# Kernel optimization log

Measured on AMD Instinct MI355X. Metric: run time of the kernel, lower is better.

## Reference

```python
import jax, jax.numpy as jnp
import numpy as np

B, N, L, C, K = 2, 8192, 8192, 128, 8
RADIUS = 0.4

def _gather(t, idx):
    # t: [B,L,D], idx: [B,N,K] -> [B,N,K,D]
    b, n, k = idx.shape
    return jnp.take_along_axis(t, idx.reshape(b, n * k)[:, :, None], axis=1).reshape(b, n, k, t.shape[-1])

def _ln(x, g, b):
    m = x.mean(-1, keepdims=True)
    v = x.var(-1, keepdims=True)
    return (x - m) * jax.lax.rsqrt(v + 1e-5) * g + b

def setup_inputs() -> dict:
    key = jax.random.key(0)
    ks = jax.random.split(key, 16)
    F = 4 * C
    def w(k, i, o):
        return jax.random.normal(k, (i, o), jnp.float32) / np.sqrt(i).astype(np.float32)
    return {
        "q_xyz": jax.random.uniform(ks[0], (B, N, 3), jnp.float32),
        "q_feat": jax.random.normal(ks[1], (B, N, C), jnp.float32),
        "kv_xyz": jax.random.uniform(ks[2], (B, L, 3), jnp.float32),
        "kv_feat": jax.random.normal(ks[3], (B, L, C), jnp.float32),
        "kv_pad": jnp.zeros((B, L), bool),
        "pos_w1": w(ks[4], 3, C), "pos_b1": jnp.zeros((C,), jnp.float32),
        "pos_w2": w(ks[5], C, C), "pos_b2": jnp.zeros((C,), jnp.float32),
        "attn_w": w(ks[6], C, C), "attn_b": jnp.zeros((C,), jnp.float32),
        "lin_w": w(ks[7], C, C),
        "lin_src_w": w(ks[8], C, C),
        "lin_dst_w": w(ks[9], C, C),
        "ln1_g": jnp.ones((C,), jnp.float32), "ln1_b": jnp.zeros((C,), jnp.float32),
        "ffn_w1": w(ks[10], C, F), "ffn_b1": jnp.zeros((F,), jnp.float32),
        "ffn_w2": w(ks[11], F, C), "ffn_b2": jnp.zeros((C,), jnp.float32),
        "ln2_g": jnp.ones((C,), jnp.float32), "ln2_b": jnp.zeros((C,), jnp.float32),
    }

def reference(q_xyz, q_feat, kv_xyz, kv_feat, kv_pad,
              pos_w1, pos_b1, pos_w2, pos_b2, attn_w, attn_b,
              lin_w, lin_src_w, lin_dst_w, ln1_g, ln1_b,
              ffn_w1, ffn_b1, ffn_w2, ffn_b2, ln2_g, ln2_b):
    # --- radius graph: up to K nearest kv points within RADIUS per query ---
    d2 = jnp.sum((q_xyz[:, :, None, :] - kv_xyz[:, None, :, :]) ** 2, -1)  # [B,N,L]
    ok = (d2 <= RADIUS ** 2) & (~kv_pad)[:, None, :]
    neg_d2, idx = jax.lax.top_k(jnp.where(ok, -d2, -jnp.inf), K)  # [B,N,K]
    ev = jnp.isfinite(neg_d2)  # edge-valid mask [B,N,K]

    # --- PointTransformerConv (vector attention, per-edge) ---
    pos_j = _gather(kv_xyz, idx)                           # [B,N,K,3]
    rel = q_xyz[:, :, None, :] - pos_j                     # pos_i - pos_j
    # pos_nn: MLP([3,C,C], plain_last=False) => ReLU after each Linear
    delta = jax.nn.relu(jax.nn.relu(rel @ pos_w1 + pos_b1) @ pos_w2 + pos_b2)  # [B,N,K,C]
    a_src = _gather(kv_feat @ lin_src_w, idx)              # [B,N,K,C]
    a_dst = q_feat @ lin_dst_w                             # [B,N,C]
    x_j = _gather(kv_feat @ lin_w, idx)                    # [B,N,K,C]
    # attn_nn: MLP([C,C], plain_last=False) => Linear + ReLU
    alpha = jax.nn.relu((a_dst[:, :, None, :] - a_src + delta) @ attn_w + attn_b)
    # segment softmax over the K neighbors (invalid edges masked out)
    scores = jnp.where(ev[..., None], alpha, -jnp.inf)
    mx = jnp.max(scores, axis=2, keepdims=True)
    mx = jnp.where(jnp.isfinite(mx), mx, 0.0)
    e = jnp.where(ev[..., None], jnp.exp(scores - mx), 0.0)
    attn = e / jnp.maximum(e.sum(2, keepdims=True), 1e-12)
    agg = jnp.sum(attn * (x_j + delta), axis=2)            # [B,N,C]

    # --- residual + LN + FFN + LN (dropout = identity at eval) ---
    out = _ln(q_feat + agg, ln1_g, ln1_b)
    h = jax.nn.gelu(out @ ffn_w1 + ffn_b1, approximate=False) @ ffn_w2 + ffn_b2
    return _ln(out + h, ln2_g, ln2_b)
```

## Files before the change

kernel.cpp:

```cpp
#include <hip/hip_runtime.h>
#include <math.h>

#define NB 2
#define NQ 8192
#define NL 8192
#define NC 128
#define NKN 8
#define NF 512
#define MQ (NB*NQ)

typedef __attribute__((ext_vector_type(8))) short bf16x8;
typedef __attribute__((ext_vector_type(4))) float f32x4;

__device__ __forceinline__ unsigned short f2bf_u(float f){
    unsigned u = __float_as_uint(f);
    return (unsigned short)((u + 0x7FFFu + ((u>>16)&1u)) >> 16);
}
__device__ __forceinline__ float bf2f(unsigned short s){
    return __uint_as_float(((unsigned)s) << 16);
}


__device__ __forceinline__ int cell_coord(float x) {
    int c = (int)(x * 16.0f);
    return min(15, max(0, c));
}

__global__ __launch_bounds__(256) void grid_count_kernel(
    const float* __restrict__ kxyz, const unsigned char* __restrict__ pad,
    int* __restrict__ cnt)
{
    int t = blockIdx.x*256 + threadIdx.x;
    if (pad[t]) return;
    int bat = t >> 13;
    float x = kxyz[t*3+0], y = kxyz[t*3+1], z = kxyz[t*3+2];
    int cell = (cell_coord(z)*16 + cell_coord(y))*16 + cell_coord(x);
    atomicAdd(&cnt[bat*4096 + cell], 1);
}

__global__ __launch_bounds__(1024) void grid_scan_kernel(
    const int* __restrict__ cnt, int* __restrict__ cs)
{
    __shared__ int wsum[17];
    int t = threadIdx.x;
    int v[8]; int s = 0;
    #pragma unroll
    for (int k = 0; k < 8; ++k) { v[k] = s; s += cnt[t*8 + k]; }
    int lane = t & 63, w = t >> 6;
    int inc = s;
    #pragma unroll
    for (int d = 1; d < 64; d <<= 1) {
        int o = __shfl_up(inc, d);
        if (lane >= d) inc += o;
    }
    if (lane == 63) wsum[w] = inc;
    __syncthreads();
    if (t == 0) {
        int a = 0;
        for (int i = 0; i < 16; ++i) { int x = wsum[i]; wsum[i] = a; a += x; }
        wsum[16] = a;
    }
    __syncthreads();
    int base = wsum[w] + (inc - s);
    #pragma unroll
    for (int k = 0; k < 8; ++k) cs[t*8 + k] = base + v[k];
    if (t == 1023) cs[8192] = wsum[16];
}

__global__ __launch_bounds__(256) void grid_scatter_kernel(
    const float* __restrict__ kxyz, const unsigned char* __restrict__ pad,
    const int* __restrict__ cs, int* __restrict__ fill, float4* __restrict__ ro)
{
    int t = blockIdx.x*256 + threadIdx.x;
    if (pad[t]) return;
    int bat = t >> 13, i = t & 8191;
    float x = kxyz[t*3+0], y = kxyz[t*3+1], z = kxyz[t*3+2];
    int cell = bat*4096 + (cell_coord(z)*16 + cell_coord(y))*16 + cell_coord(x);
    int pos = cs[cell] + atomicAdd(&fill[cell], 1);
    ro[pos] = make_float4(x, y, z, __int_as_float(i));
}

__device__ __forceinline__ void insert8(float cd, int id, float dk[8], int ik[8]) {
    if (cd < dk[7]) {
        dk[7] = cd; ik[7] = id;
        #pragma unroll
        for (int r = 6; r >= 0; --r) {
            bool sw = dk[r+1] < dk[r];
            float td = dk[r]; int ti = ik[r];
            dk[r]   = sw ? dk[r+1] : dk[r];
            ik[r]   = sw ? ik[r+1] : ik[r];
            dk[r+1] = sw ? td : dk[r+1];
            ik[r+1] = sw ? ti : ik[r+1];
        }
    }
}

template<int W>
__device__ __forceinline__ void scan_block(int l, int cx, int cy, int cz,
    float qx, float qy, float qz, const int* __restrict__ CS,
    const float4* __restrict__ RO, float dk[8], int ik[8])
{
    const int D = 2*W + 1;
    int xs = max(0, cx - W), xe = min(15, cx + W);
    int nx = xe - xs + 1;
    for (int r = l; r < D*D; r += 8) {
        int dz = r / D - W, dy = r % D - W;
        int zz = cz + dz, yy = cy + dy;
        if ((unsigned)zz > 15u || (unsigned)yy > 15u) continue;
        int c0 = (zz*16 + yy)*16 + xs;
        int s = CS[c0], e = CS[c0 + nx];
        for (int p = s; p < e; ++p) {
            float4 v = RO[p];
            float dx = qx - v.x, dyv = qy - v.y, dzv = qz - v.z;
            float cd = dx*dx + dyv*dyv + dzv*dzv;
            insert8(cd, __float_as_int(v.w), dk, ik);
        }
    }
}

__device__ __forceinline__ void merge8(float dk[8], int ik[8]) {
    #pragma unroll
    for (int m = 1; m <= 4; m <<= 1) {
        float od[8]; int oi[8];
        #pragma unroll
        for (int r = 0; r < 8; ++r) {
            od[r] = __shfl_xor(dk[r], m);
            oi[r] = __shfl_xor(ik[r], m);
        }
        float nd[8]; int ni[8];
        #pragma unroll
        for (int r = 0; r < 8; ++r) {
            bool take = od[7-r] < dk[r];
            nd[r] = take ? od[7-r] : dk[r];
            ni[r] = take ? oi[7-r] : ik[r];
        }
        #pragma unroll
        for (int st = 4; st >= 1; st >>= 1) {
            #pragma unroll
            for (int r = 0; r < 8; ++r) {
                if ((r & st) == 0 && (r | st) < 8) {
                    int b = r | st;
                    bool sw = nd[b] < nd[r];
                    float td = nd[r]; int ti = ni[r];
                    nd[r] = sw ? nd[b] : nd[r];
                    ni[r] = sw ? ni[b] : ni[r];
                    nd[b] = sw ? td : nd[b];
                    ni[b] = sw ? ti : ni[b];
                }
            }
        }
        #pragma unroll
        for (int r = 0; r < 8; ++r) { dk[r] = nd[r]; ik[r] = ni[r]; }
    }
}

__global__ __launch_bounds__(256) void radius_grid_query_kernel(
    const float* __restrict__ qxyz, const int* __restrict__ cellstart,
    const float4* __restrict__ reorder, int* __restrict__ idxout)
{
    const int tid  = threadIdx.x;
    const int l    = tid & 7;
    const int qloc = tid >> 3;
    const int gq   = blockIdx.x*32 + qloc;
    const int bat  = gq >> 13;
    const float qx = qxyz[gq*3+0], qy = qxyz[gq*3+1], qz = qxyz[gq*3+2];
    const int cx = cell_coord(qx), cy = cell_coord(qy), cz = cell_coord(qz);
    const int* CS = cellstart + bat*4096;
    const float R2  = (float)(0.4*0.4);
    const float R2P = __uint_as_float(__float_as_uint(R2) + 1u);

    float dk[8]; int ik[8];
    #pragma unroll
    for (int r = 0; r < 8; ++r) { dk[r] = R2P; ik[r] = -1; }

    scan_block<2>(l, cx, cy, cz, qx, qy, qz, CS, reorder, dk, ik);
    merge8(dk, ik);
    bool done = dk[7] <= 0.015625f;

    if (!done) {
        #pragma unroll
        for (int r = 0; r < 8; ++r) { dk[r] = R2P; ik[r] = -1; }
        scan_block<4>(l, cx, cy, cz, qx, qy, qz, CS, reorder, dk, ik);
        merge8(dk, ik);
        done = dk[7] <= 0.0625f;
    }
    if (!done) {
        #pragma unroll
        for (int r = 0; r < 8; ++r) { dk[r] = R2P; ik[r] = -1; }
        scan_block<16>(l, cx, cy, cz, qx, qy, qz, CS, reorder, dk, ik);
        merge8(dk, ik);
    }

    if (l == 0) {
        int o[8];
        #pragma unroll
        for (int r = 0; r < 8; ++r) o[r] = (dk[r] <= R2) ? ik[r] : -1;
        int4 a = {o[0], o[1], o[2], o[3]};
        int4 b = {o[4], o[5], o[6], o[7]};
        *(int4*)&idxout[(size_t)gq*8 + 0] = a;
        *(int4*)&idxout[(size_t)gq*8 + 4] = b;
    }
}

__global__ __launch_bounds__(256) void prep_all_kernel(
    const float* __restrict__ posw2, const float* __restrict__ attnw,
    const float* __restrict__ lin_w, const float* __restrict__ lin_src_w,
    const float* __restrict__ lin_dst_w,
    const float* __restrict__ ffn_w1, const float* __restrict__ ffn_w2,
    unsigned short* __restrict__ imgb, int* __restrict__ zero_p)
{
    int t = blockIdx.x*256 + threadIdx.x;
    if (t < 16384) {
        int k = t >> 7, n = t & 127;
        imgb[(k >> 5)*4096 + n*32 + (k & 31)] = f2bf_u(posw2[t]);
    } else if (t < 32768) {
        int u = t - 16384;
        int k = u >> 7, n = u & 127;
        imgb[16384 + (k >> 5)*4096 + n*32 + (k & 31)] = f2bf_u(attnw[u]);
    } else if (t < 65536) {
        int u = t - 32768;
        int k = u >> 8, n = u & 255;
        float v = (n < 128) ? lin_w[k*128 + n] : lin_src_w[k*128 + (n-128)];
        imgb[32768 + ((k >> 5)*256 + n)*32 + (k & 31)] = f2bf_u(v);
    } else if (t < 81920) {
        int u = t - 65536;
        int k = u >> 7, n = u & 127;
        imgb[65536 + ((k >> 5)*128 + n)*32 + (k & 31)] = f2bf_u(lin_dst_w[u]);
    } else if (t < 147456) {
        int u = t - 81920;
        int k = u >> 9, n = u & 511;
        imgb[81920 + ((k >> 5)*512 + n)*32 + (k & 31)] = f2bf_u(ffn_w1[u]);
    } else if (t < 212992) {
        int u = t - 147456;
        int k = u >> 7, n = u & 127;
        imgb[147456 + ((k >> 5)*128 + n)*32 + (k & 31)] = f2bf_u(ffn_w2[u]);
    } else {
        zero_p[t - 212992] = 0;
    }
}

__global__ __launch_bounds__(256) void lin3_kernel(
    const float* __restrict__ kv_feat, const float* __restrict__ q_feat,
    const unsigned short* __restrict__ wvs, const unsigned short* __restrict__ wd,
    unsigned short* __restrict__ vs, float* __restrict__ adst)
{
    __shared__ unsigned short sA[64*32];
    __shared__ unsigned short sB[128*32];
    const int tid = threadIdx.x;
    const int w = tid >> 6, lane = tid & 63, l15 = lane & 15, quad = lane >> 4;
    const int row0 = blockIdx.x*64;
    const int y = blockIdx.y;
    const float* A = (y == 2) ? q_feat : kv_feat;
    const unsigned short* Bimg = (y == 2) ? wd : wvs;
    const int BNd = (y == 2) ? 128 : 256;
    const int col0 = (y == 2) ? 0 : y*128;

    f32x4 acc[8];
    #pragma unroll
    for (int t=0;t<8;t++){ acc[t][0]=0.f; acc[t][1]=0.f; acc[t][2]=0.f; acc[t][3]=0.f; }

    for (int kc = 0; kc < 4; ++kc) {
        __syncthreads();
        #pragma unroll
        for (int it = 0; it < 2; ++it) {
            int ix = it*256 + tid;
            int r = ix >> 3, kq = ix & 7;
            float4 a4 = *(const float4*)&A[(size_t)(row0+r)*NC + kc*32 + kq*4];
            ushort4 pk = { f2bf_u(a4.x), f2bf_u(a4.y), f2bf_u(a4.z), f2bf_u(a4.w) };
            *(ushort4*)&sA[r*32 + kq*4] = pk;
        }
        const int4* bsrc = (const int4*)(Bimg + ((size_t)kc*BNd + col0)*32);
        #pragma unroll
        for (int it = 0; it < 2; ++it) {
            int o = it*256 + tid;
            ((int4*)sB)[o] = bsrc[o];
        }
        __syncthreads();
        bf16x8 af = *(const bf16x8*)&sA[(w*16 + l15)*32 + quad*8];
        #pragma unroll
        for (int t = 0; t < 8; ++t) {
            bf16x8 bf = *(const bf16x8*)&sB[(16*t + l15)*32 + quad*8];
            acc[t] = __builtin_amdgcn_mfma_f32_16x16x32_bf16(af, bf, acc[t], 0, 0, 0);
        }
    }

    const int rowb = row0 + w*16 + quad*4;
    #pragma unroll
    for (int t = 0; t < 8; ++t) {
        int col = col0 + 16*t + l15;
        #pragma unroll
        for (int r = 0; r < 4; ++r) {
            if (y == 2) adst[(size_t)(rowb+r)*NC + col] = acc[t][r];
            else        vs[(size_t)(rowb+r)*256 + col] = f2bf_u(acc[t][r]);
        }
    }
}

__device__ inline float gelu_exact(float x) {
    return 0.5f*x*(1.0f + erff(x*0.7071067811865476f));
}

__global__ __launch_bounds__(128) void ffn_fused_kernel(
    const float* __restrict__ in1,
    const unsigned short* __restrict__ wf1, const unsigned short* __restrict__ wf2,
    const float* __restrict__ b1v, const float* __restrict__ b2v,
    const float* __restrict__ g, const float* __restrict__ bb,
    float* __restrict__ out)
{
    __shared__ unsigned short sA[16*136];
    __shared__ unsigned short sH[2*16*136];
    __shared__ float sR[16*132];
    const int tid = threadIdx.x;
    const int w = tid >> 6, lane = tid & 63, l15 = lane & 15, quad = lane >> 4;
    const int row0 = blockIdx.x*16;

    #pragma unroll
    for (int it = 0; it < 4; ++it) {
        int ix = it*128 + tid;
        int r = ix >> 5, kq = ix & 31;
        float4 a4 = *(const float4*)&in1[(size_t)(row0+r)*NC + kq*4];
        ushort4 pk = { f2bf_u(a4.x), f2bf_u(a4.y), f2bf_u(a4.z), f2bf_u(a4.w) };
        *(ushort4*)&sA[r*136 + kq*4] = pk;
    }
    __syncthreads();

    bf16x8 af[4];
    #pragma unroll
    for (int kk=0;kk<4;kk++)
        af[kk] = *(const bf16x8*)&sA[l15*136 + kk*32 + quad*8];

    f32x4 acc2[8];
    #pragma unroll
    for (int t=0;t<8;t++){ acc2[t][0]=0.f; acc2[t][1]=0.f; acc2[t][2]=0.f; acc2[t][3]=0.f; }

    unsigned short* Hw = sH + w*16*136;

    #pragma unroll
    for (int ci = 0; ci < 2; ++ci) {
        const int c = w*2 + ci;
        f32x4 acc1[8];
        #pragma unroll
        for (int t=0;t<8;t++){ acc1[t][0]=0.f; acc1[t][1]=0.f; acc1[t][2]=0.f; acc1[t][3]=0.f; }
        #pragma unroll
        for (int kk=0;kk<4;kk++){
            #pragma unroll
            for (int t=0;t<8;t++){
                int n = c*128 + 16*t + l15;
                bf16x8 bf = *(const bf16x8*)&wf1[((size_t)kk*512 + n)*32 + quad*8];
                acc1[t] = __builtin_amdgcn_mfma_f32_16x16x32_bf16(af[kk], bf, acc1[t], 0, 0, 0);
            }
        }
        #pragma unroll
        for (int t=0;t<8;t++){
            float bv = b1v[c*128 + 16*t + l15];
            #pragma unroll
            for (int r=0;r<4;r++){
                float x = gelu_exact(acc1[t][r] + bv);
                Hw[(quad*4+r)*136 + 16*t + l15] = f2bf_u(x);
            }
        }
        __syncthreads();
        #pragma unroll
        for (int kk=0;kk<4;kk++){
            bf16x8 a2 = *(const bf16x8*)&Hw[l15*136 + kk*32 + quad*8];
            #pragma unroll
            for (int t=0;t<8;t++){
                bf16x8 bf = *(const bf16x8*)&wf2[((size_t)((c*4+kk)*128) + 16*t + l15)*32 + quad*8];
                acc2[t] = __builtin_amdgcn_mfma_f32_16x16x32_bf16(a2, bf, acc2[t], 0, 0, 0);
            }
        }
        __syncthreads();
    }

    if (w == 1) {
        #pragma unroll
        for (int t=0;t<8;t++)
            #pragma unroll
            for (int r=0;r<4;r++)
                sR[(quad*4+r)*132 + 16*t + l15] = acc2[t][r];
    }
    __syncthreads();
    if (w == 0) {
        #pragma unroll
        for (int r = 0; r < 4; ++r) {
            int row = row0 + quad*4 + r;
            float xv[8]; float S = 0.f;
            #pragma unroll
            for (int t = 0; t < 8; ++t) {
                int col = 16*t + l15;
                float a = acc2[t][r] + sR[(quad*4+r)*132 + col];
                xv[t] = a + b2v[col] + in1[(size_t)row*NC + col];
                S += xv[t];
            }
            #pragma unroll
            for (int m = 1; m <= 8; m <<= 1) S += __shfl_xor(S, m);
            float mean = S * (1.f/128.f);
            float V = 0.f;
            #pragma unroll
            for (int t = 0; t < 8; ++t) { float d = xv[t]-mean; V += d*d; }
            #pragma unroll
            for (int m = 1; m <= 8; m <<= 1) V += __shfl_xor(V, m);
            float rstd = rsqrtf(V*(1.f/128.f) + 1e-5f);
            #pragma unroll
            for (int t = 0; t < 8; ++t) {
                int col = 16*t + l15;
                out[(size_t)row*NC + col] = (xv[t]-mean)*rstd*g[col] + bb[col];
            }
        }
    }
}

__global__ __launch_bounds__(256) void attn_mfma_kernel(
    const float* __restrict__ qxyz, const float* __restrict__ qfeat,
    const float* __restrict__ kxyz,
    const float* __restrict__ posw1, const float* __restrict__ posb1,
    const float* __restrict__ posb2, const float* __restrict__ attnb,
    const float* __restrict__ ln1g, const float* __restrict__ ln1b,
    const unsigned short* __restrict__ wimg1, const unsigned short* __restrict__ wimg2,
    const int* __restrict__ idx, const unsigned short* __restrict__ vs,
    const float* __restrict__ adst, float* __restrict__ out1)
{
    __shared__ unsigned short s_w[16384];
    __shared__ unsigned short s_V[4*16*136];
    __shared__ unsigned short s_T[4*16*136];
    __shared__ float s_w1[384];
    __shared__ float s_b1[128], s_b2[128], s_ab[128], s_g[128], s_bb[128];
    __shared__ int   s_j[64];

    const int tid  = threadIdx.x;
    const int w    = tid >> 6;
    const int lane = tid & 63;
    const int l15  = lane & 15;
    const int quad = lane >> 4;
    const int qbase = blockIdx.x*8 + w*2;
    const int bat  = (blockIdx.x*8) >> 13;

    if (tid < 128) {
        s_b1[tid] = posb1[tid]; s_b2[tid] = posb2[tid];
        s_ab[tid] = attnb[tid]; s_g[tid] = ln1g[tid]; s_bb[tid] = ln1b[tid];
    } else {
        int i = tid - 128;
        s_w1[i] = posw1[i]; s_w1[128+i] = posw1[128+i]; s_w1[256+i] = posw1[256+i];
    }
    if (tid < 64) s_j[tid] = idx[(size_t)blockIdx.x*64 + tid];
    #pragma unroll
    for (int r = 0; r < 8; ++r)
        ((int4*)s_w)[r*256 + tid] = ((const int4*)wimg1)[r*256 + tid];
    __syncthreads();

    #pragma unroll
    for (int i = 0; i < 4; ++i) {
        int ix = lane + i*64;
        int el = ix >> 4, c16 = ix & 15;
        int j = s_j[w*16 + el];
        int jc = j < 0 ? 0 : j;
        const int4* rp = (const int4*)(vs + ((size_t)(bat*NL + jc))*256);
        int dst = (w*16 + el)*136 + c16*8;
        *(int4*)&s_V[dst] = rp[c16];
        *(int4*)&s_T[dst] = rp[16 + c16];
    }

    bf16x8 h1f[4];
    {
        int e  = w*16 + l15;
        int qh = qbase + (l15 >> 3);
        int j  = s_j[e];
        int jc = j < 0 ? 0 : j;
        const float* kp = kxyz + ((size_t)(bat*NL + jc))*3;
        float rx = qxyz[qh*3+0]-kp[0], ry = qxyz[qh*3+1]-kp[1], rz = qxyz[qh*3+2]-kp[2];
        #pragma unroll
        for (int kk=0;kk<4;kk++){
            #pragma unroll
            for (int jj=0;jj<8;jj++){
                int c = kk*32 + quad*8 + jj;
                float h = s_b1[c] + rx*s_w1[c] + ry*s_w1[128+c] + rz*s_w1[256+c];
                h = fmaxf(h, 0.f);
                h1f[kk][jj] = (short)f2bf_u(h);
            }
        }
    }

    f32x4 acc[8];
    #pragma unroll
    for (int t=0;t<8;t++){ acc[t][0]=0.f; acc[t][1]=0.f; acc[t][2]=0.f; acc[t][3]=0.f; }
    #pragma unroll
    for (int kk=0;kk<4;kk++){
        #pragma unroll
        for (int t=0;t<8;t++){
            bf16x8 wf = *(const bf16x8*)&s_w[kk*4096 + (16*t + l15)*32 + quad*8];
            acc[t] = __builtin_amdgcn_mfma_f32_16x16x32_bf16(h1f[kk], wf, acc[t], 0, 0, 0);
        }
    }

    f32x4 dreg[8];
    #pragma unroll
    for (int t=0;t<8;t++){
        float b2v = s_b2[16*t + l15];
        #pragma unroll
        for (int r=0;r<4;r++) dreg[t][r] = fmaxf(acc[t][r] + b2v, 0.f);
    }

    int jr[4]; bool val[4];
    #pragma unroll
    for (int r=0;r<4;r++){
        int j = s_j[w*16 + quad*4 + r];
        val[r] = (j >= 0); jr[r] = j < 0 ? 0 : j;
    }
    const int qt = qbase + (quad >> 1);
    float ad[8];
    #pragma unroll
    for (int t=0;t<8;t++) ad[t] = adst[(size_t)qt*NC + 16*t + l15];

    __syncthreads();

    #pragma unroll
    for (int r = 0; r < 8; ++r)
        ((int4*)s_w)[r*256 + tid] = ((const int4*)wimg2)[r*256 + tid];

    {
        unsigned short* st = s_T + w*16*136;
        #pragma unroll
        for (int t=0;t<8;t++){
            #pragma unroll
            for (int r=0;r<4;r++){
                int o = (quad*4 + r)*136 + 16*t + l15;
                float sv = bf2f(st[o]);
                st[o] = f2bf_u(ad[t] - sv + dreg[t][r]);
            }
        }
    }
    __syncthreads();

    f32x4 acc2[8];
    #pragma unroll
    for (int t=0;t<8;t++){ acc2[t][0]=0.f; acc2[t][1]=0.f; acc2[t][2]=0.f; acc2[t][3]=0.f; }
    {
        const unsigned short* st = s_T + w*16*136;
        #pragma unroll
        for (int kk=0;kk<4;kk++){
            bf16x8 tf = *(const bf16x8*)&st[l15*136 + kk*32 + quad*8];
            #pragma unroll
            for (int t=0;t<8;t++){
                bf16x8 wf = *(const bf16x8*)&s_w[kk*4096 + (16*t + l15)*32 + quad*8];
                acc2[t] = __builtin_amdgcn_mfma_f32_16x16x32_bf16(tf, wf, acc2[t], 0, 0, 0);
            }
        }
    }

    float ex[8][4]; float dnm[8];
    #pragma unroll
    for (int t=0;t<8;t++){
        float ab = s_ab[16*t + l15];
        float s0 = val[0] ? fmaxf(acc2[t][0] + ab, 0.f) : -INFINITY;
        float s1 = val[1] ? fmaxf(acc2[t][1] + ab, 0.f) : -INFINITY;
        float s2 = val[2] ? fmaxf(acc2[t][2] + ab, 0.f) : -INFINITY;
        float s3 = val[3] ? fmaxf(acc2[t][3] + ab, 0.f) : -INFINITY;
        float mx = fmaxf(fmaxf(s0,s1), fmaxf(s2,s3));
        mx = fmaxf(mx, __shfl_xor(mx, 16));
        if (mx < -1e37f) mx = 0.f;
        ex[t][0] = __expf(s0 - mx);
        ex[t][1] = __expf(s1 - mx);
        ex[t][2] = __expf(s2 - mx);
        ex[t][3] = __expf(s3 - mx);
        float sm = ex[t][0]+ex[t][1]+ex[t][2]+ex[t][3];
        sm += __shfl_xor(sm, 16);
        dnm[t] = fmaxf(sm, 1e-12f);
    }

    float part[8];
    #pragma unroll
    for (int t=0;t<8;t++){
        float p = 0.f;
        #pragma unroll
        for (int r=0;r<4;r++){
            float vv = bf2f(s_V[(w*16 + quad*4 + r)*136 + 16*t + l15]);
            p += ex[t][r] * (vv + dreg[t][r]);
        }
        p += __shfl_xor(p, 16);
        part[t] = p / dnm[t];
    }

    float xln[8];
    float S = 0.f;
    #pragma unroll
    for (int t=0;t<8;t++){
        xln[t] = qfeat[(size_t)qt*NC + 16*t + l15] + part[t];
        S += xln[t];
    }
    #pragma unroll
    for (int m=1;m<=8;m<<=1) S += __shfl_xor(S, m);
    float mean = S * (1.f/128.f);
    float V = 0.f;
    #pragma unroll
    for (int t=0;t<8;t++){ float d = xln[t]-mean; V += d*d; }
    #pragma unroll
    for (int m=1;m<=8;m<<=1) V += __shfl_xor(V, m);
    float rstd = rsqrtf(V*(1.f/128.f) + 1e-5f);

    if ((quad & 1) == 0){
        #pragma unroll
        for (int t=0;t<8;t++){
            int c = 16*t + l15;
            out1[(size_t)qt*NC + c] = (xln[t]-mean)*rstd*s_g[c] + s_bb[c];
        }
    }
}

extern "C" void kernel_launch(void* const* d_in, const int* in_sizes, int n_in,
                              void* d_out, int out_size, void* d_ws, size_t ws_size,
                              hipStream_t stream)
{
    (void)in_sizes; (void)n_in; (void)out_size; (void)ws_size;
    const float* q_xyz   = (const float*)d_in[0];
    const float* q_feat  = (const float*)d_in[1];
    const float* kv_xyz  = (const float*)d_in[2];
    const float* kv_feat = (const float*)d_in[3];
    const unsigned char* kv_pad = (const unsigned char*)d_in[4];
    const float* pos_w1  = (const float*)d_in[5];
    const float* pos_b1  = (const float*)d_in[6];
    const float* pos_w2  = (const float*)d_in[7];
    const float* pos_b2  = (const float*)d_in[8];
    const float* attn_w  = (const float*)d_in[9];
    const float* attn_b  = (const float*)d_in[10];
    const float* lin_w   = (const float*)d_in[11];
    const float* lin_src_w = (const float*)d_in[12];
    const float* lin_dst_w = (const float*)d_in[13];
    const float* ln1_g   = (const float*)d_in[14];
    const float* ln1_b   = (const float*)d_in[15];
    const float* ffn_w1  = (const float*)d_in[16];
    const float* ffn_b1  = (const float*)d_in[17];
    const float* ffn_w2  = (const float*)d_in[18];
    const float* ffn_b2  = (const float*)d_in[19];
    const float* ln2_g   = (const float*)d_in[20];
    const float* ln2_b   = (const float*)d_in[21];

    float* ws    = (float*)d_ws;
    int*   idx   = (int*)d_ws;
    unsigned short* vs = (unsigned short*)(ws + 131072);
    float* adst  = ws + 131072 + 2*2097152;
    float* out1  = adst + 2097152;
    float* Hreg  = out1 + 2097152;

    float4* reorder  = (float4*)Hreg;
    int* cellcnt   = (int*)(reorder + 16384);
    int* cellfill  = cellcnt + 8192;
    int* cellstart = cellfill + 8192;

    unsigned short* imgb  = (unsigned short*)((char*)Hreg + (1u << 20));
    unsigned short* wimg1 = imgb;
    unsigned short* wimg2 = imgb + 16384;
    unsigned short* wvs   = imgb + 32768;
    unsigned short* wd    = imgb + 65536;
    unsigned short* wf1   = imgb + 81920;
    unsigned short* wf2   = imgb + 147456;

    prep_all_kernel<<<dim3(896), dim3(256), 0, stream>>>(
        pos_w2, attn_w, lin_w, lin_src_w, lin_dst_w, ffn_w1, ffn_w2, imgb, cellcnt);

    grid_count_kernel<<<dim3(64), dim3(256), 0, stream>>>(kv_xyz, kv_pad, cellcnt);
    grid_scan_kernel<<<dim3(1), dim3(1024), 0, stream>>>(cellcnt, cellstart);
    grid_scatter_kernel<<<dim3(64), dim3(256), 0, stream>>>(kv_xyz, kv_pad, cellstart, cellfill, reorder);
    radius_grid_query_kernel<<<dim3(MQ/32), dim3(256), 0, stream>>>(q_xyz, cellstart, reorder, idx);

    lin3_kernel<<<dim3(MQ/64, 3), dim3(256), 0, stream>>>(kv_feat, q_feat, wvs, wd, vs, adst);

    attn_mfma_kernel<<<dim3(MQ/8), dim3(256), 0, stream>>>(
        q_xyz, q_feat, kv_xyz,
        pos_w1, pos_b1, pos_b2, attn_b, ln1_g, ln1_b,
        wimg1, wimg2, idx, vs, adst, out1);

    ffn_fused_kernel<<<dim3(MQ/16), dim3(128), 0, stream>>>(
        out1, wf1, wf2, ffn_b1, ffn_b2, ln2_g, ln2_b, (float*)d_out);
}
```

Baseline: 235.6 us.

## Split FFN block across four waves with column-partitioned second GEMM

The fused FFN kernel moves from 2 waves to 4 waves per 16-row block. Each wave now computes one 128-column chunk of the hidden layer. For the second GEMM each wave owns 32 output columns and reads the whole GELU hidden tile from shared memory, instead of every wave accumulating all 128 columns and doing a cross-wave reduction. The A operand is loaded straight from global memory into registers, and LayerNorm now uses single-pass sum and sum-of-squares statistics reduced through shared memory. The aim is more parallelism and fewer syncs and accumulator registers, at the cost of the variance formula being less numerically stable.

```diff
diff --git a/kernel.cpp b/kernel.cpp
--- a/kernel.cpp
+++ b/kernel.cpp
@@ -300,112 +300,134 @@
     return 0.5f*x*(1.0f + erff(x*0.7071067811865476f));
 }
 
-__global__ __launch_bounds__(128) void ffn_fused_kernel(
+__global__ __launch_bounds__(256, 4) void ffn_fused_kernel(
     const float* __restrict__ in1,
     const unsigned short* __restrict__ wf1, const unsigned short* __restrict__ wf2,
     const float* __restrict__ b1v, const float* __restrict__ b2v,
     const float* __restrict__ g, const float* __restrict__ bb,
     float* __restrict__ out)
 {
-    __shared__ unsigned short sA[16*136];
-    __shared__ unsigned short sH[2*16*136];
-    __shared__ float sR[16*132];
+    __shared__ unsigned short sH[4*16*136];
+    __shared__ float4 sS[16];
+    __shared__ float4 sQ[16];
     const int tid = threadIdx.x;
     const int w = tid >> 6, lane = tid & 63, l15 = lane & 15, quad = lane >> 4;
     const int row0 = blockIdx.x*16;
 
-    #pragma unroll
-    for (int it = 0; it < 4; ++it) {
-        int ix = it*128 + tid;
-        int r = ix >> 5, kq = ix & 31;
-        float4 a4 = *(const float4*)&in1[(size_t)(row0+r)*NC + kq*4];
-        ushort4 pk = { f2bf_u(a4.x), f2bf_u(a4.y), f2bf_u(a4.z), f2bf_u(a4.w) };
-        *(ushort4*)&sA[r*136 + kq*4] = pk;
-    }
-    __syncthreads();
-
     bf16x8 af[4];
-    #pragma unroll
-    for (int kk=0;kk<4;kk++)
-        af[kk] = *(const bf16x8*)&sA[l15*136 + kk*32 + quad*8];
-
-    f32x4 acc2[8];
-    #pragma unroll
-    for (int t=0;t<8;t++){ acc2[t][0]=0.f; acc2[t][1]=0.f; acc2[t][2]=0.f; acc2[t][3]=0.f; }
-
-    unsigned short* Hw = sH + w*16*136;
-
-    #pragma unroll
-    for (int ci = 0; ci < 2; ++ci) {
-        const int c = w*2 + ci;
-        f32x4 acc1[8];
-        #pragma unroll
-        for (int t=0;t<8;t++){ acc1[t][0]=0.f; acc1[t][1]=0.f; acc1[t][2]=0.f; acc1[t][3]=0.f; }
-        #pragma unroll
-        for (int kk=0;kk<4;kk++){
-            #pragma unroll
-            for (int t=0;t<8;t++){
-                int n = c*128 + 16*t + l15;
-                bf16x8 bf = *(const bf16x8*)&wf1[((size_t)kk*512 + n)*32 + quad*8];
-                acc1[t] = __builtin_amdgcn_mfma_f32_16x16x32_bf16(af[kk], bf, acc1[t], 0, 0, 0);
-            }
-        }
+    {
+        const float* arow = in1 + (size_t)(row0 + l15)*NC;
+        #pragma unroll
+        for (int kk = 0; kk < 4; ++kk) {
+            float4 a0 = *(const float4*)&arow[kk*32 + quad*8];
+            float4 a1 = *(const float4*)&arow[kk*32 + quad*8 + 4];
+            bf16x8 v;
+            v[0]=(short)f2bf_u(a0.x); v[1]=(short)f2bf_u(a0.y);
+            v[2]=(short)f2bf_u(a0.z); v[3]=(short)f2bf_u(a0.w);
+            v[4]=(short)f2bf_u(a1.x); v[5]=(short)f2bf_u(a1.y);
+            v[6]=(short)f2bf_u(a1.z); v[7]=(short)f2bf_u(a1.w);
+            af[kk] = v;
+        }
+    }
+
+    f32x4 acc1[8];
+    #pragma unroll
+    for (int t=0;t<8;t++){ acc1[t][0]=0.f; acc1[t][1]=0.f; acc1[t][2]=0.f; acc1[t][3]=0.f; }
+    #pragma unroll
+    for (int kk=0;kk<4;kk++){
         #pragma unroll
         for (int t=0;t<8;t++){
-            float bv = b1v[c*128 + 16*t + l15];
+            int n = w*128 + 16*t + l15;
+            bf16x8 bf = *(const bf16x8*)&wf1[((size_t)kk*512 + n)*32 + quad*8];
+            acc1[t] = __builtin_amdgcn_mfma_f32_16x16x32_bf16(af[kk], bf, acc1[t], 0, 0, 0);
+        }
+    }
+
+    {
+        unsigned short* Hw = sH + w*(16*136);
+        #pragma unroll
+        for (int t=0;t<8;t++){
+            float bv = b1v[w*128 + 16*t + l15];
             #pragma unroll
             for (int r=0;r<4;r++){
                 float x = gelu_exact(acc1[t][r] + bv);
                 Hw[(quad*4+r)*136 + 16*t + l15] = f2bf_u(x);
             }
         }
-        __syncthreads();
-        #pragma unroll
-        for (int kk=0;kk<4;kk++){
-            bf16x8 a2 = *(const bf16x8*)&Hw[l15*136 + kk*32 + quad*8];
-            #pragma unroll
-            for (int t=0;t<8;t++){
-                bf16x8 bf = *(const bf16x8*)&wf2[((size_t)((c*4+kk)*128) + 16*t + l15)*32 + quad*8];
-                acc2[t] = __builtin_amdgcn_mfma_f32_16x16x32_bf16(a2, bf, acc2[t], 0, 0, 0);
-            }
-        }
-        __syncthreads();
-    }
-
-    if (w == 1) {
-        #pragma unroll
-        for (int t=0;t<8;t++)
-            #pragma unroll
-            for (int r=0;r<4;r++)
-                sR[(quad*4+r)*132 + 16*t + l15] = acc2[t][r];
     }
     __syncthreads();
-    if (w == 0) {
-        #pragma unroll
-        for (int r = 0; r < 4; ++r) {
+
+    f32x4 acc2[2];
+    #pragma unroll
+    for (int tt=0;tt<2;tt++){ acc2[tt][0]=0.f; acc2[tt][1]=0.f; acc2[tt][2]=0.f; acc2[tt][3]=0.f; }
+    #pragma unroll
+    for (int kkg=0;kkg<16;kkg++){
+        const unsigned short* Ht = sH + (kkg>>2)*(16*136);
+        bf16x8 a2 = *(const bf16x8*)&Ht[l15*136 + (kkg&3)*32 + quad*8];
+        #pragma unroll
+        for (int tt=0;tt<2;tt++){
+            int col = (2*w+tt)*16 + l15;
+            bf16x8 bf = *(const bf16x8*)&wf2[((size_t)kkg*128 + col)*32 + quad*8];
+            acc2[tt] = __builtin_amdgcn_mfma_f32_16x16x32_bf16(a2, bf, acc2[tt], 0, 0, 0);
+        }
+    }
+
+    float xv[2][4];
+    float S0=0.f,S1=0.f,S2=0.f,S3=0.f;
+    float Q0=0.f,Q1=0.f,Q2=0.f,Q3=0.f;
+    #pragma unroll
+    for (int tt=0;tt<2;tt++){
+        int col = (2*w+tt)*16 + l15;
+        float bv = b2v[col];
+        #pragma unroll
+        for (int r=0;r<4;r++){
             int row = row0 + quad*4 + r;
-            float xv[8]; float S = 0.f;
-            #pragma unroll
-            for (int t = 0; t < 8; ++t) {
-                int col = 16*t + l15;
-                float a = acc2[t][r] + sR[(quad*4+r)*132 + col];
-                xv[t] = a + b2v[col] + in1[(size_t)row*NC + col];
-                S += xv[t];
-            }
-            #pragma unroll
-            for (int m = 1; m <= 8; m <<= 1) S += __shfl_xor(S, m);
-            float mean = S * (1.f/128.f);
-            float V = 0.f;
-            #pragma unroll
-            for (int t = 0; t < 8; ++t) { float d = xv[t]-mean; V += d*d; }
-            #pragma unroll
-            for (int m = 1; m <= 8; m <<= 1) V += __shfl_xor(V, m);
-            float rstd = rsqrtf(V*(1.f/128.f) + 1e-5f);
-            #pragma unroll
-            for (int t = 0; t < 8; ++t) {
-                int col = 16*t + l15;
-                out[(size_t)row*NC + col] = (xv[t]-mean)*rstd*g[col] + bb[col];
-            }
+            float x = acc2[tt][r] + bv + in1[(size_t)row*NC + col];
+            xv[tt][r] = x;
+            if (r==0){ S0+=x; Q0+=x*x; } else if (r==1){ S1+=x; Q1+=x*x; }
+            else if (r==2){ S2+=x; Q2+=x*x; } else { S3+=x; Q3+=x*x; }
+        }
+    }
+    #pragma unroll
+    for (int m=1;m<=8;m<<=1){
+        S0 += __shfl_xor(S0,m); S1 += __shfl_xor(S1,m);
+        S2 += __shfl_xor(S2,m); S3 += __shfl_xor(S3,m);
+        Q0 += __shfl_xor(Q0,m); Q1 += __shfl_xor(Q1,m);
+        Q2 += __shfl_xor(Q2,m); Q3 += __shfl_xor(Q3,m);
+    }
+    if (l15 == 0){
+        sS[w*4 + quad] = make_float4(S0,S1,S2,S3);
+        sQ[w*4 + quad] = make_float4(Q0,Q1,Q2,Q3);
+    }
+    __syncthreads();
+
+    float4 St = sS[quad]; float4 Qt = sQ[quad];
+    {
+        float4 a = sS[4+quad],  b = sS[8+quad],  c = sS[12+quad];
+        St.x += a.x+b.x+c.x; St.y += a.y+b.y+c.y; St.z += a.z+b.z+c.z; St.w += a.w+b.w+c.w;
+        float4 d = sQ[4+quad], e = sQ[8+quad],  f = sQ[12+quad];
+        Qt.x += d.x+e.x+f.x; Qt.y += d.y+e.y+f.y; Qt.z += d.z+e.z+f.z; Qt.w += d.w+e.w+f.w;
+    }
+    float mean[4], rstd[4];
+    {
+        float sv[4] = {St.x, St.y, St.z, St.w};
+        float qv[4] = {Qt.x, Qt.y, Qt.z, Qt.w};
+        #pragma unroll
+        for (int r=0;r<4;r++){
+            float m_ = sv[r]*(1.f/128.f);
+            float v_ = qv[r]*(1.f/128.f) - m_*m_;
+            mean[r] = m_;
+            rstd[r] = rsqrtf(v_ + 1e-5f);
+        }
+    }
+    #pragma unroll
+    for (int tt=0;tt<2;tt++){
+        int col = (2*w+tt)*16 + l15;
+        float gv = g[col], bv = bb[col];
+        #pragma unroll
+        for (int r=0;r<4;r++){
+            int row = row0 + quad*4 + r;
+            out[(size_t)row*NC + col] = (xv[tt][r]-mean[r])*rstd[r]*gv + bv;
         }
     }
 }
@@ -669,6 +691,6 @@
         pos_w1, pos_b1, pos_b2, attn_b, ln1_g, ln1_b,
         wimg1, wimg2, idx, vs, adst, out1);
 
-    ffn_fused_kernel<<<dim3(MQ/16), dim3(128), 0, stream>>>(
+    ffn_fused_kernel<<<dim3(MQ/16), dim3(256), 0, stream>>>(
         out1, wf1, wf2, ffn_b1, ffn_b2, ln2_g, ln2_b, (float*)d_out);
 }
```

Measured after the change: 219.7 us (median of 2 runs). -6.8%, faster.
